# Kernel optimization log

Hardware: AMD Instinct MI355X
Metric: run time of the kernel (lower is better)

Reference implementation:

```python
import jax, jax.numpy as jnp
import numpy as np

B, L, E = 8, 512, 256
H = W = 128
NH = 8
HD = E // NH


def setup_inputs() -> dict:
    key = jax.random.key(0)
    ks = jax.random.split(key, 8)
    return {
        "query_row": jax.random.normal(ks[0], (B, L, E), jnp.float32),
        "query_col": jax.random.normal(ks[1], (B, L, E), jnp.float32),
        "key_row": jax.random.normal(ks[2], (B, H, W, E), jnp.float32),
        "key_col": jax.random.normal(ks[3], (B, H, W, E), jnp.float32),
        "value": jax.random.normal(ks[4], (B, H, W, E), jnp.float32),
        "in_proj_weight": jax.random.normal(ks[5], (5 * E, E), jnp.float32) * 0.02,
        "in_proj_bias": jnp.zeros((5 * E,), jnp.float32),
        "out_proj_weight": jax.random.normal(ks[6], (E, E), jnp.float32) * 0.02,
        "out_proj_bias": jnp.zeros((E,), jnp.float32),
    }


def reference(query_row, query_col, key_row, key_col, value,
              in_proj_weight, in_proj_bias, out_proj_weight, out_proj_bias):
    b, tgt_len, embed_dim = query_row.shape
    h, w = key_col.shape[1], key_row.shape[2]
    nh, hd = NH, embed_dim // NH
    scale = float(hd) ** -0.5

    def proj(x, i):
        Wi = in_proj_weight[i * embed_dim:(i + 1) * embed_dim]
        bi = in_proj_bias[i * embed_dim:(i + 1) * embed_dim]
        return x @ Wi.T + bi

    q_row = proj(query_row, 0) * scale            # [B,L,E]
    q_col = proj(query_col, 1) * scale            # [B,L,E]
    k_row = proj(key_row, 2).mean(axis=1)         # mean over H -> [B,W,E]
    k_col = proj(key_col, 3).mean(axis=2)         # mean over W -> [B,H,E]
    v = proj(value, 4)                            # [B,H,W,E]

    def heads(x):  # [..., E] -> [B, nh, ..., hd]
        return x.reshape(x.shape[:-1] + (nh, hd))

    q_row_h = heads(q_row).transpose(0, 2, 1, 3)        # [B,nh,L,hd]
    q_col_h = heads(q_col).transpose(0, 2, 1, 3)        # [B,nh,L,hd]
    k_row_h = heads(k_row).transpose(0, 2, 1, 3)        # [B,nh,W,hd]
    k_col_h = heads(k_col).transpose(0, 2, 1, 3)        # [B,nh,H,hd]
    v_h = heads(v).transpose(0, 3, 1, 2, 4)             # [B,nh,H,W,hd]

    a_row = jax.nn.softmax(jnp.einsum('bnld,bnwd->bnlw', q_row_h, k_row_h), axis=-1)
    a_col = jax.nn.softmax(jnp.einsum('bnld,bnhd->bnlh', q_col_h, k_col_h), axis=-1)

    # contract over H first, then over W (matches torch's src_len_col >= src_len_row branch)
    ao_col = jnp.einsum('bnlh,bnhwc->bnlwc', a_col, v_h)      # [B,nh,L,W,hd]
    out = jnp.einsum('bnlw,bnlwc->bnlc', a_row, ao_col)       # [B,nh,L,hd]

    out = out.transpose(2, 0, 1, 3).reshape(tgt_len, b, embed_dim)  # [L,B,E]
    return out @ out_proj_weight.T + out_proj_bias
```

## Files before the change

### kernel.cpp

```cpp
#include <hip/hip_runtime.h>
#include <stdint.h>

#define B_  8
#define L_  512
#define E_  256
#define H_  128
#define W_  128
#define NH_ 8
#define HD_ 32

typedef unsigned short ushort_t;
typedef __attribute__((ext_vector_type(8))) short bf16x8;
typedef __attribute__((ext_vector_type(4))) float f32x4;

__device__ __forceinline__ float bf2f(ushort_t u) {
    union { unsigned int i; float f; } x;
    x.i = ((unsigned int)u) << 16;
    return x.f;
}
__device__ __forceinline__ ushort_t f2bf(float f) {
    union { float f; unsigned int i; } x;
    x.f = f;
    unsigned int r = x.i + 0x7FFFu + ((x.i >> 16) & 1u);
    return (ushort_t)(r >> 16);
}

__global__ __launch_bounds__(256) void mean_h_kernel(const float* __restrict__ kr,
                                                     float* __restrict__ out) {
    int i = blockIdx.x * 256 + threadIdx.x;
    int e = i & (E_ - 1);
    int w = (i >> 8) & (W_ - 1);
    int b = i >> 15;
    const float* p = kr + ((size_t)b * H_ * W_ + w) * E_ + e;
    float s = 0.f;
    for (int h = 0; h < H_; ++h) s += p[(size_t)h * W_ * E_];
    out[i] = s * (1.0f / H_);
}
__global__ __launch_bounds__(256) void mean_w_kernel(const float* __restrict__ kc,
                                                     float* __restrict__ out) {
    int i = blockIdx.x * 256 + threadIdx.x;
    int e = i & (E_ - 1);
    int h = (i >> 8) & (H_ - 1);
    int b = i >> 15;
    const float* p = kc + ((size_t)(b * H_ + h) * W_) * E_ + e;
    float s = 0.f;
    for (int w = 0; w < W_; ++w) s += p[(size_t)w * E_];
    out[i] = s * (1.0f / W_);
}

__device__ __forceinline__ void load4f(const float* p, float* v) {
    float4 t = *(const float4*)p;
    v[0] = t.x; v[1] = t.y; v[2] = t.z; v[3] = t.w;
}
__device__ __forceinline__ void store4(float* p, float a, float b, float c, float d) {
    float4 t; t.x = a; t.y = b; t.z = c; t.w = d;
    *(float4*)p = t;
}

__global__ __launch_bounds__(256) void gemm256(const float* __restrict__ A,
                                               const float* __restrict__ Wt,
                                               const float* __restrict__ bias,
                                               float* __restrict__ C, int M, float scale) {
    __shared__ __align__(16) float As[16][64];
    __shared__ __align__(16) float Bs[16][64];
    const int m0 = blockIdx.x * 64;
    const int n0 = blockIdx.y * 64;
    const int tid = threadIdx.x;
    const int lr = tid >> 2;
    const int lk = (tid & 3) << 2;
    const int tx = tid & 15, ty = tid >> 4;
    float acc[4][4] = {{0.f}};

    for (int k0 = 0; k0 < E_; k0 += 16) {
        float av[4], wv[4];
        load4f(A + (size_t)(m0 + lr) * E_ + k0 + lk, av);
        load4f(Wt + (size_t)(n0 + lr) * E_ + k0 + lk, wv);
        As[lk + 0][lr] = av[0]; As[lk + 1][lr] = av[1];
        As[lk + 2][lr] = av[2]; As[lk + 3][lr] = av[3];
        Bs[lk + 0][lr] = wv[0]; Bs[lk + 1][lr] = wv[1];
        Bs[lk + 2][lr] = wv[2]; Bs[lk + 3][lr] = wv[3];
        __syncthreads();
#pragma unroll
        for (int k = 0; k < 16; ++k) {
            float a[4], b[4];
            load4f(&As[k][ty << 2], a);
            load4f(&Bs[k][tx << 2], b);
#pragma unroll
            for (int i = 0; i < 4; ++i)
#pragma unroll
                for (int j = 0; j < 4; ++j) acc[i][j] += a[i] * b[j];
        }
        __syncthreads();
    }
    float bv[4];
    load4f(bias + n0 + (tx << 2), bv);
#pragma unroll
    for (int i = 0; i < 4; ++i) {
        float* cp = C + (size_t)(m0 + (ty << 2) + i) * E_ + n0 + (tx << 2);
        store4(cp, scale * (acc[i][0] + bv[0]), scale * (acc[i][1] + bv[1]),
                   scale * (acc[i][2] + bv[2]), scale * (acc[i][3] + bv[3]));
    }
}

__global__ __launch_bounds__(256) void wconv_kernel(const float* __restrict__ w,
                                                    ushort_t* __restrict__ wbf) {
    int i = (blockIdx.x * 256 + threadIdx.x) * 4;
    float4 f = *(const float4*)(w + i);
    ushort4 u;
    u.x = f2bf(f.x); u.y = f2bf(f.y); u.z = f2bf(f.z); u.w = f2bf(f.w);
    *(ushort4*)(wbf + i) = u;
}

#define KP_ 264
__global__ __launch_bounds__(256) void vproj_mfma(const float* __restrict__ Ag,
                                                  const ushort_t* __restrict__ Wbf,
                                                  const float* __restrict__ bias,
                                                  ushort_t* __restrict__ v_t) {
    __shared__ ushort_t A_lds[64 * KP_];
    const int m0 = blockIdx.x * 64;
    const int tid = threadIdx.x, lane = tid & 63, wv = tid >> 6;
    const int quad = lane >> 4, lc = lane & 15;
    {
        int r = tid >> 2, kq = (tid & 3) * 64;
        const float* sa = Ag + (size_t)(m0 + r) * 256 + kq;
        ushort_t* da = A_lds + r * KP_ + kq;
#pragma unroll
        for (int j = 0; j < 16; ++j) {
            float4 f = *(const float4*)(sa + j * 4);
            ushort4 u;
            u.x = f2bf(f.x); u.y = f2bf(f.y); u.z = f2bf(f.z); u.w = f2bf(f.w);
            *(ushort4*)(da + j * 4) = u;
        }
    }
    __syncthreads();

    f32x4 acc[4][4];
#pragma unroll
    for (int t = 0; t < 4; ++t)
#pragma unroll
        for (int et = 0; et < 4; ++et) {
            acc[t][et][0] = 0.f; acc[t][et][1] = 0.f;
            acc[t][et][2] = 0.f; acc[t][et][3] = 0.f;
        }

    const ushort_t* wrow = Wbf + (size_t)(wv * 64 + lc) * 256 + quad * 8;

#pragma unroll
    for (int kc = 0; kc < 8; ++kc) {
        bf16x8 vf[4];
#pragma unroll
        for (int t = 0; t < 4; ++t)
            vf[t] = *(const bf16x8*)(A_lds + (t * 16 + lc) * KP_ + kc * 32 + quad * 8);
#pragma unroll
        for (int et = 0; et < 4; ++et) {
            bf16x8 wf = *(const bf16x8*)(wrow + (size_t)(et * 16) * 256 + kc * 32);
#pragma unroll
            for (int t = 0; t < 4; ++t)
                acc[t][et] = __builtin_amdgcn_mfma_f32_16x16x32_bf16(vf[t], wf, acc[t][et], 0, 0, 0);
        }
    }

    const int b = m0 >> 14;
    const int ml = m0 & 16383;
    ushort_t* vtb = v_t + (size_t)b * 4194304 + ml + quad * 4;
#pragma unroll
    for (int et = 0; et < 4; ++et) {
        const int e = wv * 64 + et * 16 + lc;
        const float bv = bias[e];
        ushort_t* vte = vtb + (size_t)e * 16384;
#pragma unroll
        for (int t = 0; t < 4; ++t) {
            ushort4 u;
            u.x = f2bf(acc[t][et][0] + bv);
            u.y = f2bf(acc[t][et][1] + bv);
            u.z = f2bf(acc[t][et][2] + bv);
            u.w = f2bf(acc[t][et][3] + bv);
            *(ushort4*)(vte + t * 16) = u;
        }
    }
}

__global__ __launch_bounds__(256) void scores_row(const float* __restrict__ q,
                                                  const float* __restrict__ k,
                                                  float* __restrict__ a) {
    const int lt = blockIdx.x, bn = blockIdx.y;
    const int n = bn & 7, b = bn >> 3;
    const int tid = threadIdx.x;
    __shared__ float ks[128][36];
    {
        int r = tid >> 1, c16 = (tid & 1) * 16;
        const float* src = k + ((size_t)b * 128 + r) * 256 + n * 32 + c16;
#pragma unroll
        for (int j = 0; j < 4; ++j) {
            float4 f = *(const float4*)(src + j * 4);
            ks[r][c16 + j * 4 + 0] = f.x; ks[r][c16 + j * 4 + 1] = f.y;
            ks[r][c16 + j * 4 + 2] = f.z; ks[r][c16 + j * 4 + 3] = f.w;
        }
    }
    const int ll = tid >> 3, wq = tid & 7;
    float4 q4r[8];
    {
        const float* qp = q + ((size_t)b * 512 + lt * 32 + ll) * 256 + n * 32;
#pragma unroll
        for (int c4 = 0; c4 < 8; ++c4) q4r[c4] = *(const float4*)(qp + c4 * 4);
    }
    __syncthreads();
    float dots[16];
#pragma unroll
    for (int j = 0; j < 16; ++j) dots[j] = 0.f;
#pragma unroll
    for (int c4 = 0; c4 < 8; ++c4) {
        float4 q4 = q4r[c4];
#pragma unroll
        for (int j = 0; j < 16; ++j) {
            float4 k4 = *(const float4*)&ks[j * 8 + wq][c4 * 4];
            dots[j] += q4.x * k4.x + q4.y * k4.y + q4.z * k4.z + q4.w * k4.w;
        }
    }
    float mx = dots[0];
#pragma unroll
    for (int j = 1; j < 16; ++j) mx = fmaxf(mx, dots[j]);
    for (int d = 1; d < 8; d <<= 1) mx = fmaxf(mx, __shfl_xor(mx, d, 64));
    float ex[16], sm = 0.f;
#pragma unroll
    for (int j = 0; j < 16; ++j) { ex[j] = __expf(dots[j] - mx); sm += ex[j]; }
    for (int d = 1; d < 8; d <<= 1) sm += __shfl_xor(sm, d, 64);
    float inv = 1.0f / sm;
    float* ap = a + ((size_t)bn * 512 + lt * 32 + ll) * 128 + wq;
#pragma unroll
    for (int j = 0; j < 16; ++j) ap[j * 8] = ex[j] * inv;
}

__global__ __launch_bounds__(256) void scores_col(const float* __restrict__ q,
                                                  const float* __restrict__ k,
                                                  float* __restrict__ ac_t) {
    const int lt = blockIdx.x, bn = blockIdx.y;
    const int n = bn & 7, b = bn >> 3;
    const int tid = threadIdx.x;
    __shared__ float qs[32][36];
    __shared__ float sc[128][33];
    __shared__ float mxr[8][32], smr[8][32], fin[2][32];
    {
        int r = tid >> 3, c4 = (tid & 7) * 4;
        float4 f = *(const float4*)(q + ((size_t)b * 512 + lt * 32 + r) * 256 + n * 32 + c4);
        qs[r][c4 + 0] = f.x; qs[r][c4 + 1] = f.y; qs[r][c4 + 2] = f.z; qs[r][c4 + 3] = f.w;
    }
    const int h = tid >> 1, lq = tid & 1;
    float4 kk[8];
    {
        const float* kp = k + ((size_t)b * 128 + h) * 256 + n * 32;
#pragma unroll
        for (int c4 = 0; c4 < 8; ++c4) kk[c4] = *(const float4*)(kp + c4 * 4);
    }
    __syncthreads();
    float dots[16];
#pragma unroll
    for (int j = 0; j < 16; ++j) dots[j] = 0.f;
#pragma unroll
    for (int c4 = 0; c4 < 8; ++c4) {
        float4 k4 = kk[c4];
#pragma unroll
        for (int j = 0; j < 16; ++j) {
            float4 q4 = *(const float4*)&qs[j * 2 + lq][c4 * 4];
            dots[j] += k4.x * q4.x + k4.y * q4.y + k4.z * q4.z + k4.w * q4.w;
        }
    }
#pragma unroll
    for (int j = 0; j < 16; ++j) sc[h][j * 2 + lq] = dots[j];
    __syncthreads();
    {
        int lcol = tid & 31, seg = tid >> 5;
        float m = -3.0e38f;
#pragma unroll
        for (int i = 0; i < 16; ++i) m = fmaxf(m, sc[seg * 16 + i][lcol]);
        mxr[seg][lcol] = m;
    }
    __syncthreads();
    if (tid < 32) {
        float m = mxr[0][tid];
#pragma unroll
        for (int s = 1; s < 8; ++s) m = fmaxf(m, mxr[s][tid]);
        fin[0][tid] = m;
    }
    __syncthreads();
    {
        int lcol = tid & 31, seg = tid >> 5;
        float m = fin[0][lcol], s = 0.f;
#pragma unroll
        for (int i = 0; i < 16; ++i) s += __expf(sc[seg * 16 + i][lcol] - m);
        smr[seg][lcol] = s;
    }
    __syncthreads();
    if (tid < 32) {
        float t = 0.f;
#pragma unroll
        for (int s = 1; s < 8; ++s) t += smr[s][tid];
        fin[1][tid] = 1.0f / (t + smr[0][tid]);
    }
    __syncthreads();
    {
        const int lh = (tid & 1) * 16;
        float* op = ac_t + ((size_t)bn * 128 + h) * 512 + lt * 32;
#pragma unroll
        for (int j4 = 0; j4 < 4; ++j4) {
            int l0 = lh + j4 * 4;
            float4 o;
            o.x = __expf(sc[h][l0 + 0] - fin[0][l0 + 0]) * fin[1][l0 + 0];
            o.y = __expf(sc[h][l0 + 1] - fin[0][l0 + 1]) * fin[1][l0 + 1];
            o.z = __expf(sc[h][l0 + 2] - fin[0][l0 + 2]) * fin[1][l0 + 2];
            o.w = __expf(sc[h][l0 + 3] - fin[0][l0 + 3]) * fin[1][l0 + 3];
            *(float4*)(op + l0) = o;
        }
    }
}

#define ARP 136
#define VBP 136
__global__ __launch_bounds__(256) void core_mfma(const float* __restrict__ a_row,
                                                 const float* __restrict__ ac_t,
                                                 const ushort_t* __restrict__ v_t,
                                                 float* __restrict__ attn) {
    __shared__ ushort_t ar_lds[64 * ARP];
    __shared__ ushort_t vb_lds[2][64 * VBP];
    const int blk = blockIdx.x;
    const int lt = blk >> 6, bn = blk & 63;
    const int n = bn & 7, b = bn >> 3;
    const int tid = threadIdx.x, lane = tid & 63, wv = tid >> 6;
    const int quad = lane >> 4, lc = lane & 15;

    {
        const size_t abase = ((size_t)bn * L_ + lt * 64) * 128;
        int r = tid >> 2, wq = (tid & 3) * 32;
        const float* src = a_row + abase + (size_t)r * 128 + wq;
        ushort_t* dst = ar_lds + r * ARP + wq;
#pragma unroll
        for (int j = 0; j < 8; ++j) {
            float4 f = *(const float4*)(src + j * 4);
            ushort4 u;
            u.x = f2bf(f.x); u.y = f2bf(f.y); u.z = f2bf(f.z); u.w = f2bf(f.w);
            *(ushort4*)(dst + j * 4) = u;
        }
    }
    const float* act = ac_t + (size_t)bn * 65536 + lt * 64 + wv * 16 + quad * 4;
    const ushort_t* vtb = v_t + (size_t)b * 4194304 + (size_t)(n * 32) * 16384;
    const int sc_ = tid >> 3, sw = (tid & 7) * 16;
#define STAGE2(hh, bu)                                                             \
    {                                                                              \
        const ushort_t* s0 = vtb + (size_t)sc_ * 16384 + (hh) * 128 + sw;          \
        ushort_t* d0 = vb_lds[bu] + sc_ * VBP + sw;                                \
        *(uint4*)d0 = *(const uint4*)s0;                                           \
        *(uint4*)(d0 + 8) = *(const uint4*)(s0 + 8);                               \
        const ushort_t* s1 = s0 + 128;                                             \
        ushort_t* d1 = d0 + 32 * VBP;                                              \
        *(uint4*)d1 = *(const uint4*)s1;                                           \
        *(uint4*)(d1 + 8) = *(const uint4*)(s1 + 8);                               \
    }
    STAGE2(0, 0);
    __syncthreads();
    bf16x8 A[4];
#pragma unroll
    for (int kc = 0; kc < 4; ++kc)
        A[kc] = *(const bf16x8*)(ar_lds + (wv * 16 + lc) * ARP + kc * 32 + quad * 8);

    f32x4 acc0 = {0.f,0.f,0.f,0.f}, acc1 = {0.f,0.f,0.f,0.f};
    for (int hh = 0; hh < 128; hh += 2) {
        const int buf = (hh >> 1) & 1;
        if (hh) __syncthreads();
        if (hh + 2 < 128) STAGE2(hh + 2, buf ^ 1);
        float4 av0 = *(const float4*)(act + (size_t)hh * 512);
        float4 av1 = *(const float4*)(act + (size_t)(hh + 1) * 512);
        const ushort_t* vb0 = vb_lds[buf];
        const ushort_t* vb1 = vb_lds[buf] + 32 * VBP;
        f32x4 t0 = {0.f,0.f,0.f,0.f}, t1 = {0.f,0.f,0.f,0.f};
        f32x4 u0 = {0.f,0.f,0.f,0.f}, u1 = {0.f,0.f,0.f,0.f};
#pragma unroll
        for (int kc = 0; kc < 4; ++kc) {
            const int ko = kc * 32 + quad * 8;
            bf16x8 b0 = *(const bf16x8*)(vb0 + lc * VBP + ko);
            bf16x8 b1 = *(const bf16x8*)(vb0 + (16 + lc) * VBP + ko);
            bf16x8 c0 = *(const bf16x8*)(vb1 + lc * VBP + ko);
            bf16x8 c1 = *(const bf16x8*)(vb1 + (16 + lc) * VBP + ko);
            t0 = __builtin_amdgcn_mfma_f32_16x16x32_bf16(A[kc], b0, t0, 0, 0, 0);
            t1 = __builtin_amdgcn_mfma_f32_16x16x32_bf16(A[kc], b1, t1, 0, 0, 0);
            u0 = __builtin_amdgcn_mfma_f32_16x16x32_bf16(A[kc], c0, u0, 0, 0, 0);
            u1 = __builtin_amdgcn_mfma_f32_16x16x32_bf16(A[kc], c1, u1, 0, 0, 0);
        }
        acc0[0] += av0.x * t0[0] + av1.x * u0[0]; acc1[0] += av0.x * t1[0] + av1.x * u1[0];
        acc0[1] += av0.y * t0[1] + av1.y * u0[1]; acc1[1] += av0.y * t1[1] + av1.y * u1[1];
        acc0[2] += av0.z * t0[2] + av1.z * u0[2]; acc1[2] += av0.z * t1[2] + av1.z * u1[2];
        acc0[3] += av0.w * t0[3] + av1.w * u0[3]; acc1[3] += av0.w * t1[3] + av1.w * u1[3];
    }
    const int row0 = wv * 16 + quad * 4;
#pragma unroll
    for (int r = 0; r < 4; ++r) {
        size_t o = ((size_t)(lt * 64 + row0 + r) * B_ + b) * E_ + n * HD_ + lc;
        attn[o] = acc0[r];
        attn[o + 16] = acc1[r];
    }
#undef STAGE2
}

extern "C" void kernel_launch(void* const* d_in, const int* in_sizes, int n_in,
                              void* d_out, int out_size, void* d_ws, size_t ws_size,
                              hipStream_t stream) {
    const float* query_row = (const float*)d_in[0];
    const float* query_col = (const float*)d_in[1];
    const float* key_row   = (const float*)d_in[2];
    const float* key_col   = (const float*)d_in[3];
    const float* value     = (const float*)d_in[4];
    const float* ipw       = (const float*)d_in[5];
    const float* ipb       = (const float*)d_in[6];
    const float* opw       = (const float*)d_in[7];
    const float* opb       = (const float*)d_in[8];
    float* out = (float*)d_out;

    char* ws = (char*)d_ws;
    float* q_row_s = (float*)ws;  ws += (size_t)4096 * 256 * 4;
    float* q_col_s = (float*)ws;  ws += (size_t)4096 * 256 * 4;
    float* krm     = (float*)ws;  ws += (size_t)262144 * 4;
    float* kcm     = (float*)ws;  ws += (size_t)262144 * 4;
    float* k_row   = (float*)ws;  ws += (size_t)262144 * 4;
    float* k_col   = (float*)ws;  ws += (size_t)262144 * 4;
    ushort_t* v_t  = (ushort_t*)ws; ws += (size_t)33554432 * 2;
    float* a_row   = (float*)ws;  ws += (size_t)4194304 * 4;
    float* ac_t    = (float*)ws;  ws += (size_t)4194304 * 4;
    float* attn    = (float*)ws;  ws += (size_t)4096 * 256 * 4;
    ushort_t* wbf  = (ushort_t*)ws; ws += (size_t)65536 * 2;

    const float scale = 0.17677669529663687f;

    mean_h_kernel<<<1024, 256, 0, stream>>>(key_row, krm);
    mean_w_kernel<<<1024, 256, 0, stream>>>(key_col, kcm);
    wconv_kernel<<<64, 256, 0, stream>>>(ipw + 4 * 65536, wbf);

    gemm256<<<dim3(64, 4), 256, 0, stream>>>(query_row, ipw + 0 * 65536, ipb + 0,    q_row_s, 4096, scale);
    gemm256<<<dim3(64, 4), 256, 0, stream>>>(query_col, ipw + 1 * 65536, ipb + 256,  q_col_s, 4096, scale);
    gemm256<<<dim3(16, 4), 256, 0, stream>>>(krm,       ipw + 2 * 65536, ipb + 512,  k_row,   1024, 1.0f);
    gemm256<<<dim3(16, 4), 256, 0, stream>>>(kcm,       ipw + 3 * 65536, ipb + 768,  k_col,   1024, 1.0f);

    vproj_mfma<<<2048, 256, 0, stream>>>(value, wbf, ipb + 1024, v_t);

    scores_row<<<dim3(16, 64), 256, 0, stream>>>(q_row_s, k_row, a_row);
    scores_col<<<dim3(16, 64), 256, 0, stream>>>(q_col_s, k_col, ac_t);

    core_mfma<<<512, 256, 0, stream>>>(a_row, ac_t, v_t, attn);

    gemm256<<<dim3(64, 4), 256, 0, stream>>>(attn, opw, opb, out, 4096, 1.0f);
}
```

Before: 618.1 us.

## Register-prefetch V tiles and weight fragments to overlap global loads with MFMA

In core_mfma, the next V tile is now loaded from global memory into registers before the MFMA work and written to the alternate LDS buffer afterwards. This replaces the old stage-then-compute pattern, where the global load sat directly in front of the LDS store, and lets load latency hide behind compute with one barrier per iteration. vproj_mfma software-pipelines its weight fragment loads one k-chunk ahead. Both kernels gain an occupancy hint of 3 blocks per SIMD, and the mean kernels get unroll-8 pragmas, at the cost of extra register pressure and possible spills under the tighter launch bound.

```diff
diff --git a/kernel.cpp b/kernel.cpp
--- a/kernel.cpp
+++ b/kernel.cpp
@@ -33,6 +33,7 @@
     int b = i >> 15;
     const float* p = kr + ((size_t)b * H_ * W_ + w) * E_ + e;
     float s = 0.f;
+#pragma unroll 8
     for (int h = 0; h < H_; ++h) s += p[(size_t)h * W_ * E_];
     out[i] = s * (1.0f / H_);
 }
@@ -44,6 +45,7 @@
     int b = i >> 15;
     const float* p = kc + ((size_t)(b * H_ + h) * W_) * E_ + e;
     float s = 0.f;
+#pragma unroll 8
     for (int w = 0; w < W_; ++w) s += p[(size_t)w * E_];
     out[i] = s * (1.0f / W_);
 }
@@ -112,10 +114,10 @@
 }
 
 #define KP_ 264
-__global__ __launch_bounds__(256) void vproj_mfma(const float* __restrict__ Ag,
-                                                  const ushort_t* __restrict__ Wbf,
-                                                  const float* __restrict__ bias,
-                                                  ushort_t* __restrict__ v_t) {
+__global__ __launch_bounds__(256, 3) void vproj_mfma(const float* __restrict__ Ag,
+                                                     const ushort_t* __restrict__ Wbf,
+                                                     const float* __restrict__ bias,
+                                                     ushort_t* __restrict__ v_t) {
     __shared__ ushort_t A_lds[64 * KP_];
     const int m0 = blockIdx.x * 64;
     const int tid = threadIdx.x, lane = tid & 63, wv = tid >> 6;
@@ -145,19 +147,29 @@
 
     const ushort_t* wrow = Wbf + (size_t)(wv * 64 + lc) * 256 + quad * 8;
 
+    bf16x8 wf[4], wn[4];
+#pragma unroll
+    for (int et = 0; et < 4; ++et)
+        wf[et] = *(const bf16x8*)(wrow + (size_t)(et * 16) * 256);
+
 #pragma unroll
     for (int kc = 0; kc < 8; ++kc) {
         bf16x8 vf[4];
 #pragma unroll
         for (int t = 0; t < 4; ++t)
             vf[t] = *(const bf16x8*)(A_lds + (t * 16 + lc) * KP_ + kc * 32 + quad * 8);
-#pragma unroll
-        for (int et = 0; et < 4; ++et) {
-            bf16x8 wf = *(const bf16x8*)(wrow + (size_t)(et * 16) * 256 + kc * 32);
+        if (kc < 7) {
+#pragma unroll
+            for (int et = 0; et < 4; ++et)
+                wn[et] = *(const bf16x8*)(wrow + (size_t)(et * 16) * 256 + (kc + 1) * 32);
+        }
+#pragma unroll
+        for (int et = 0; et < 4; ++et)
 #pragma unroll
             for (int t = 0; t < 4; ++t)
-                acc[t][et] = __builtin_amdgcn_mfma_f32_16x16x32_bf16(vf[t], wf, acc[t][et], 0, 0, 0);
-        }
+                acc[t][et] = __builtin_amdgcn_mfma_f32_16x16x32_bf16(vf[t], wf[et], acc[t][et], 0, 0, 0);
+#pragma unroll
+        for (int et = 0; et < 4; ++et) wf[et] = wn[et];
     }
 
     const int b = m0 >> 14;
@@ -316,10 +328,10 @@
 
 #define ARP 136
 #define VBP 136
-__global__ __launch_bounds__(256) void core_mfma(const float* __restrict__ a_row,
-                                                 const float* __restrict__ ac_t,
-                                                 const ushort_t* __restrict__ v_t,
-                                                 float* __restrict__ attn) {
+__global__ __launch_bounds__(256, 3) void core_mfma(const float* __restrict__ a_row,
+                                                    const float* __restrict__ ac_t,
+                                                    const ushort_t* __restrict__ v_t,
+                                                    float* __restrict__ attn) {
     __shared__ ushort_t ar_lds[64 * ARP];
     __shared__ ushort_t vb_lds[2][64 * VBP];
     const int blk = blockIdx.x;
@@ -328,6 +340,19 @@
     const int tid = threadIdx.x, lane = tid & 63, wv = tid >> 6;
     const int quad = lane >> 4, lc = lane & 15;
 
+    const ushort_t* vtb = v_t + (size_t)b * 4194304 + (size_t)(n * 32) * 16384;
+    const int sc_ = tid >> 3, sw = (tid & 7) * 16;
+
+    uint4 p0, p1, p2, p3;
+    {
+        const ushort_t* s0 = vtb + (size_t)sc_ * 16384 + sw;
+        p0 = *(const uint4*)s0;
+        p1 = *(const uint4*)(s0 + 8);
+        const ushort_t* s1 = s0 + 128;
+        p2 = *(const uint4*)s1;
+        p3 = *(const uint4*)(s1 + 8);
+    }
+
     {
         const size_t abase = ((size_t)bn * L_ + lt * 64) * 128;
         int r = tid >> 2, wq = (tid & 3) * 32;
@@ -341,32 +366,33 @@
             *(ushort4*)(dst + j * 4) = u;
         }
     }
+    {
+        ushort_t* d0 = vb_lds[0] + sc_ * VBP + sw;
+        *(uint4*)d0 = p0;
+        *(uint4*)(d0 + 8) = p1;
+        ushort_t* d1 = d0 + 32 * VBP;
+        *(uint4*)d1 = p2;
+        *(uint4*)(d1 + 8) = p3;
+    }
+    __syncthreads();
+
     const float* act = ac_t + (size_t)bn * 65536 + lt * 64 + wv * 16 + quad * 4;
-    const ushort_t* vtb = v_t + (size_t)b * 4194304 + (size_t)(n * 32) * 16384;
-    const int sc_ = tid >> 3, sw = (tid & 7) * 16;
-#define STAGE2(hh, bu)                                                             \
-    {                                                                              \
-        const ushort_t* s0 = vtb + (size_t)sc_ * 16384 + (hh) * 128 + sw;          \
-        ushort_t* d0 = vb_lds[bu] + sc_ * VBP + sw;                                \
-        *(uint4*)d0 = *(const uint4*)s0;                                           \
-        *(uint4*)(d0 + 8) = *(const uint4*)(s0 + 8);                               \
-        const ushort_t* s1 = s0 + 128;                                             \
-        ushort_t* d1 = d0 + 32 * VBP;                                              \
-        *(uint4*)d1 = *(const uint4*)s1;                                           \
-        *(uint4*)(d1 + 8) = *(const uint4*)(s1 + 8);                               \
-    }
-    STAGE2(0, 0);
-    __syncthreads();
     bf16x8 A[4];
 #pragma unroll
     for (int kc = 0; kc < 4; ++kc)
         A[kc] = *(const bf16x8*)(ar_lds + (wv * 16 + lc) * ARP + kc * 32 + quad * 8);
 
     f32x4 acc0 = {0.f,0.f,0.f,0.f}, acc1 = {0.f,0.f,0.f,0.f};
-    for (int hh = 0; hh < 128; hh += 2) {
-        const int buf = (hh >> 1) & 1;
-        if (hh) __syncthreads();
-        if (hh + 2 < 128) STAGE2(hh + 2, buf ^ 1);
+    for (int i = 0; i < 64; ++i) {
+        const int hh = i * 2, buf = i & 1;
+        if (i < 63) {
+            const ushort_t* s0 = vtb + (size_t)sc_ * 16384 + (hh + 2) * 128 + sw;
+            p0 = *(const uint4*)s0;
+            p1 = *(const uint4*)(s0 + 8);
+            const ushort_t* s1 = s0 + 128;
+            p2 = *(const uint4*)s1;
+            p3 = *(const uint4*)(s1 + 8);
+        }
         float4 av0 = *(const float4*)(act + (size_t)hh * 512);
         float4 av1 = *(const float4*)(act + (size_t)(hh + 1) * 512);
         const ushort_t* vb0 = vb_lds[buf];
@@ -389,6 +415,15 @@
         acc0[1] += av0.y * t0[1] + av1.y * u0[1]; acc1[1] += av0.y * t1[1] + av1.y * u1[1];
         acc0[2] += av0.z * t0[2] + av1.z * u0[2]; acc1[2] += av0.z * t1[2] + av1.z * u1[2];
         acc0[3] += av0.w * t0[3] + av1.w * u0[3]; acc1[3] += av0.w * t1[3] + av1.w * u1[3];
+        if (i < 63) {
+            ushort_t* d0 = vb_lds[buf ^ 1] + sc_ * VBP + sw;
+            *(uint4*)d0 = p0;
+            *(uint4*)(d0 + 8) = p1;
+            ushort_t* d1 = d0 + 32 * VBP;
+            *(uint4*)d1 = p2;
+            *(uint4*)(d1 + 8) = p3;
+            __syncthreads();
+        }
     }
     const int row0 = wv * 16 + quad * 4;
 #pragma unroll
@@ -397,7 +432,6 @@
         attn[o] = acc0[r];
         attn[o + 16] = acc1[r];
     }
-#undef STAGE2
 }
 
 extern "C" void kernel_launch(void* const* d_in, const int* in_sizes, int n_in,
```

Measured after the change: 595.0 us. -3.7%, faster.
